# Optimization experiments

Measured on AMD Instinct MI355X. Metric: run time of the kernel, lower is better.

## Reference

```python
import jax, jax.numpy as jnp
import numpy as np


def _minplus(x, W):
    # x: [B, in], W: [out, in] -> y[b,i] = min_j (x[b,j] + W[i,j])
    return jnp.min(x[:, None, :] + W[None, :, :], axis=-1)


def _maxbplus(x, W, b):
    # x: [B, in], W: [out, in], b: [out] -> y[b,i] = max_j (x[b,j] + W[i,j]) + b[i]
    return jnp.max(x[:, None, :] + W[None, :, :], axis=-1) + b


def _basic_block(x, w1, w2, b2, sw1=None, sw2=None, sb2=None):
    out = _maxbplus(_minplus(x, w1), w2, b2)
    sc = x if sw1 is None else _maxbplus(_minplus(x, sw1), sw2, sb2)
    return jnp.minimum(out, sc)


def setup_inputs() -> dict:
    key = jax.random.key(0)
    B, IN, OUT = 1024, 256, 512
    ks = jax.random.split(key, 16)
    s = 0.05
    inp = {
        'x': jax.random.normal(ks[0], (B, IN), jnp.float32),
        # layers 1-3: in==out==IN, no block shortcut params
        'l1_w1': jax.random.normal(ks[1], (IN, IN), jnp.float32) * s,
        'l1_w2': jax.random.normal(ks[2], (IN, IN), jnp.float32) * s,
        'l1_b2': jax.random.normal(ks[3], (IN,), jnp.float32) * s,
        'l2_w1': jax.random.normal(ks[4], (IN, IN), jnp.float32) * s,
        'l2_w2': jax.random.normal(ks[5], (IN, IN), jnp.float32) * s,
        'l2_b2': jax.random.normal(ks[6], (IN,), jnp.float32) * s,
        'l3_w1': jax.random.normal(ks[7], (IN, IN), jnp.float32) * s,
        'l3_w2': jax.random.normal(ks[8], (IN, IN), jnp.float32) * s,
        'l3_b2': jax.random.normal(ks[9], (IN,), jnp.float32) * s,
        # layer 4: IN -> OUT, has block-level shortcut
        'l4_w1': jax.random.normal(ks[10], (OUT, IN), jnp.float32) * s,
        'l4_w2': jax.random.normal(ks[11], (OUT, OUT), jnp.float32) * s,
        'l4_b2': jax.random.normal(ks[12], (OUT,), jnp.float32) * s,
        'l4_sw1': jax.random.normal(ks[13], (OUT, IN), jnp.float32) * s,
        'l4_sw2': jax.random.normal(ks[14], (OUT, OUT), jnp.float32) * s,
        'l4_sb2': jax.random.normal(ks[15], (OUT,), jnp.float32) * s,
    }
    k2 = jax.random.split(jax.random.fold_in(key, 1), 3)
    inp['sc_w1'] = jax.random.normal(k2[0], (OUT, IN), jnp.float32) * s
    inp['sc_w2'] = jax.random.normal(k2[1], (OUT, OUT), jnp.float32) * s
    inp['sc_b2'] = jax.random.normal(k2[2], (OUT,), jnp.float32) * s
    return inp


def reference(x, l1_w1, l1_w2, l1_b2, l2_w1, l2_w2, l2_b2,
              l3_w1, l3_w2, l3_b2, l4_w1, l4_w2, l4_b2,
              l4_sw1, l4_sw2, l4_sb2, sc_w1, sc_w2, sc_b2):
    out = _basic_block(x, l1_w1, l1_w2, l1_b2)            # layer1 (IN->IN)
    out = _basic_block(out, l2_w1, l2_w2, l2_b2)          # layer2
    out = _basic_block(out, l3_w1, l3_w2, l3_b2)          # layer3
    out = _basic_block(out, l4_w1, l4_w2, l4_b2,
                       l4_sw1, l4_sw2, l4_sb2)            # layer4 (IN->OUT)
    sc = _maxbplus(_minplus(x, sc_w1), sc_w2, sc_b2)      # bottleneck shortcut
    return jnp.maximum(out, sc)
```

## Files before the change

kernel.cpp:

```cpp
#include <hip/hip_runtime.h>
#include <math.h>


typedef _Float16 h2 __attribute__((ext_vector_type(2)));
typedef _Float16 h8 __attribute__((ext_vector_type(8)));

template<int M, typename V> __device__ __forceinline__ V rdv(V a, V b) {
    if constexpr (M) return __builtin_elementwise_max(a, b);
    else             return __builtin_elementwise_min(a, b);
}
template<int M> __device__ __forceinline__ _Float16 rd1(_Float16 a, _Float16 b) {
    if constexpr (M) return a > b ? a : b;
    else             return a < b ? a : b;
}
#define XS(v, I0, I1) __builtin_shufflevector(v, v, I0, I1)

struct NetP {
    const float* x;
    const h8 *w11, *w12, *w21, *w22, *w31, *w32;
    const h8 *w41, *w42, *sw1, *sw2, *scw1, *scw2;
    const _Float16 *b12, *b22, *b32, *b42, *sb2, *scb2;
    float* out;
};

template<int ISMAX, int R, int K, bool GOUT>
__device__ __forceinline__ void stage(
    const h8* __restrict__ Wc,
    const _Float16* __restrict__ bias,
    const _Float16* __restrict__ X,
    const _Float16* __restrict__ E1,
    const _Float16* __restrict__ E2,
    _Float16* __restrict__ Y,
    float* __restrict__ gout, int b0,
    _Float16* __restrict__ part)
{
    constexpr int NRG = R / 4;
    constexpr int KS  = 512 / NRG;
    constexpr int NC  = (K / 8) / KS;
    static_assert(NRG * KS == 512, "thread mapping");
    const int tid  = threadIdx.x;
    const int rowg = tid & (NRG - 1);
    const int kq   = tid / NRG;
    const int kc0  = kq * NC;

    const h8* Xc0 = (const h8*)X + kc0;
    const h8* Xc1 = (const h8*)(X + K) + kc0;

    h2 a00, a01, a10, a11, a20, a21, a30, a31;

#define RDA(a, b) rdv<ISMAX>((a), (b))
#define PIECE(J0, J1)                                                   \
    {   h2 xa_ = XS(xa, J0, J1), xb_ = XS(xb, J0, J1); h2 t;            \
        t = XS(w0, J0, J1); a00 = RDA(a00, xa_ + t); a01 = RDA(a01, xb_ + t); \
        t = XS(w1, J0, J1); a10 = RDA(a10, xa_ + t); a11 = RDA(a11, xb_ + t); \
        t = XS(w2, J0, J1); a20 = RDA(a20, xa_ + t); a21 = RDA(a21, xb_ + t); \
        t = XS(w3, J0, J1); a30 = RDA(a30, xa_ + t); a31 = RDA(a31, xb_ + t); }

    {
        h8 xa = Xc0[0], xb = Xc1[0];
        const h8* Wr = Wc + (size_t)kc0 * R + rowg;
        h8 w0 = Wr[0], w1 = Wr[NRG], w2 = Wr[2 * NRG], w3 = Wr[3 * NRG];
        {   h2 xa_ = XS(xa, 0, 1), xb_ = XS(xb, 0, 1); h2 t;
            t = XS(w0, 0, 1); a00 = xa_ + t; a01 = xb_ + t;
            t = XS(w1, 0, 1); a10 = xa_ + t; a11 = xb_ + t;
            t = XS(w2, 0, 1); a20 = xa_ + t; a21 = xb_ + t;
            t = XS(w3, 0, 1); a30 = xa_ + t; a31 = xb_ + t;
        }
        PIECE(2, 3) PIECE(4, 5) PIECE(6, 7)
    }
#pragma unroll 2
    for (int kc = 1; kc < NC; ++kc) {
        h8 xa = Xc0[kc], xb = Xc1[kc];
        const h8* Wr = Wc + (size_t)(kc0 + kc) * R + rowg;
        h8 w0 = Wr[0], w1 = Wr[NRG], w2 = Wr[2 * NRG], w3 = Wr[3 * NRG];
        PIECE(0, 1) PIECE(2, 3) PIECE(4, 5) PIECE(6, 7)
    }
#undef PIECE

    h8 v8;
    v8[0] = rd1<ISMAX>(a00[0], a00[1]); v8[1] = rd1<ISMAX>(a01[0], a01[1]);
    v8[2] = rd1<ISMAX>(a10[0], a10[1]); v8[3] = rd1<ISMAX>(a11[0], a11[1]);
    v8[4] = rd1<ISMAX>(a20[0], a20[1]); v8[5] = rd1<ISMAX>(a21[0], a21[1]);
    v8[6] = rd1<ISMAX>(a30[0], a30[1]); v8[7] = rd1<ISMAX>(a31[0], a31[1]);

    if (kq) *(h8*)(part + ((size_t)(kq - 1) * NRG + rowg) * 8) = v8;
    __syncthreads();
    if (kq == 0) {
#pragma unroll
        for (int qq = 0; qq < KS - 1; ++qq)
            v8 = rdv<ISMAX>(v8, *(const h8*)(part + ((size_t)qq * NRG + rowg) * 8));

#pragma unroll
        for (int i = 0; i < 4; ++i) {
            const int r = rowg + i * NRG;
            _Float16 oc0 = v8[2 * i], oc1 = v8[2 * i + 1];
            if (ISMAX) { _Float16 bi = bias[r]; oc0 += bi; oc1 += bi; }
            if (E1) {
                _Float16 e0 = E1[r], e1 = E1[R + r];
                oc0 = oc0 < e0 ? oc0 : e0; oc1 = oc1 < e1 ? oc1 : e1;
            }
            if (E2) {
                _Float16 e0 = E2[r], e1 = E2[R + r];
                oc0 = oc0 > e0 ? oc0 : e0; oc1 = oc1 > e1 ? oc1 : e1;
            }
            if constexpr (GOUT) {
                gout[(size_t)(b0 + 0) * 512 + r] = (float)oc0;
                gout[(size_t)(b0 + 1) * 512 + r] = (float)oc1;
            } else {
                Y[r] = oc0; Y[R + r] = oc1;
            }
        }
    }
#undef RDA
    __syncthreads();
}

__global__ __launch_bounds__(512) void netf(NetP p)
{
    __shared__ __align__(16) _Float16 X0[2 * 256];
    __shared__ __align__(16) _Float16 B0[2 * 512], B1[2 * 512];
    __shared__ __align__(16) _Float16 B2[2 * 512], B3[2 * 512];
    __shared__ __align__(16) _Float16 part[3584];
    const int tid = threadIdx.x;
    const int b0  = blockIdx.x * 2;

    {
        const int bl = tid >> 8;
        const int k  = tid & 255;
        X0[bl * 256 + k] = (_Float16)p.x[(size_t)(b0 + bl) * 256 + k];
    }
    __syncthreads();

    float* o = p.out;
    stage<0,512,256,false>(p.scw1, nullptr, X0, nullptr, nullptr, B0, o, b0, part);
    stage<1,512,512,false>(p.scw2, p.scb2,  B0, nullptr, nullptr, B1, o, b0, part);
    stage<0,256,256,false>(p.w11, nullptr, X0, nullptr, nullptr, B0, o, b0, part);
    stage<1,256,256,false>(p.w12, p.b12,   B0, X0,      nullptr, B2, o, b0, part);
    stage<0,256,256,false>(p.w21, nullptr, B2, nullptr, nullptr, B0, o, b0, part);
    stage<1,256,256,false>(p.w22, p.b22,   B0, B2,      nullptr, B3, o, b0, part);
    stage<0,256,256,false>(p.w31, nullptr, B3, nullptr, nullptr, B0, o, b0, part);
    stage<1,256,256,false>(p.w32, p.b32,   B0, B3,      nullptr, B2, o, b0, part);
    stage<0,512,256,false>(p.w41, nullptr, B2, nullptr, nullptr, B0, o, b0, part);
    stage<0,512,256,false>(p.sw1, nullptr, B2, nullptr, nullptr, B3, o, b0, part);
    stage<1,512,512,false>(p.w42, p.b42,   B0, nullptr, nullptr, B2, o, b0, part);
    stage<1,512,512,true >(p.sw2, p.sb2,   B3, B2,      B1, nullptr, o, b0, part);
}

struct Prep {
    const float* s[12]; h8* d[12]; int R[12]; int K[12];
    const float* bs[6]; _Float16* bd[6]; int bn[6];
};
__global__ __launch_bounds__(256) void cvtw(Prep p)
{
    const int m = blockIdx.y;
    if (m == 12) {
        if (blockIdx.x != 0) return;
        for (int s = 0; s < 6; ++s)
            for (int i = threadIdx.x; i < p.bn[s]; i += 256)
                p.bd[s][i] = (_Float16)p.bs[s][i];
        return;
    }
    const int R = p.R[m], K = p.K[m];
    const int tilesR = R >> 6;
    const int nt = tilesR * (K >> 6);
    const int t = blockIdx.x;
    if (t >= nt) return;
    const int tr = t % tilesR, tk = t / tilesR;

    __shared__ float s[64][65];
    const int lane = threadIdx.x & 63, ty = threadIdx.x >> 6;
    const float* src = p.s[m];
#pragma unroll
    for (int r = ty; r < 64; r += 4)
        s[r][lane] = src[(size_t)(tr * 64 + r) * K + tk * 64 + lane];
    __syncthreads();
    h8* dst = p.d[m];
#pragma unroll
    for (int c = 0; c < 2; ++c) {
        int cc = ty + c * 4;
        h8 v;
#pragma unroll
        for (int j = 0; j < 8; ++j) v[j] = (_Float16)s[lane][cc * 8 + j];
        dst[(size_t)(tk * 8 + cc) * R + tr * 64 + lane] = v;
    }
}

extern "C" void kernel_launch(void* const* d_in, const int* in_sizes, int n_in,
                              void* d_out, int out_size, void* d_ws, size_t ws_size,
                              hipStream_t stream) {
    (void)in_sizes; (void)n_in; (void)ws_size; (void)out_size;
    const float* fin[19];
    for (int i = 0; i < 19; ++i) fin[i] = (const float*)d_in[i];

    _Float16* hw = (_Float16*)d_ws;

    _Float16* w11c  = hw;
    _Float16* w12c  = hw + 65536;
    _Float16* w21c  = hw + 131072;
    _Float16* w22c  = hw + 196608;
    _Float16* w31c  = hw + 262144;
    _Float16* w32c  = hw + 327680;
    _Float16* w41c  = hw + 393216;
    _Float16* w42c  = hw + 524288;
    _Float16* sw1c  = hw + 786432;
    _Float16* sw2c  = hw + 917504;
    _Float16* scw1c = hw + 1179648;
    _Float16* scw2c = hw + 1310720;
    _Float16* bia   = hw + 1572864;
    _Float16* b12 = bia, *b22 = bia + 256, *b32 = bia + 512;
    _Float16* b42 = bia + 768, *sb2 = bia + 1280, *scb2 = bia + 1792;

    Prep cw;
    const float* wsrc[12] = {fin[1], fin[2], fin[4], fin[5], fin[7], fin[8],
                             fin[10], fin[11], fin[13], fin[14], fin[16], fin[17]};
    _Float16* wdst[12]    = {w11c, w12c, w21c, w22c, w31c, w32c,
                             w41c, w42c, sw1c, sw2c, scw1c, scw2c};
    const int wR[12] = {256,256,256,256,256,256, 512,512,512,512,512,512};
    const int wK[12] = {256,256,256,256,256,256, 256,512,256,512,256,512};
    for (int i = 0; i < 12; ++i) {
        cw.s[i] = wsrc[i]; cw.d[i] = (h8*)wdst[i]; cw.R[i] = wR[i]; cw.K[i] = wK[i];
    }
    const float* bsrc[6] = {fin[3], fin[6], fin[9], fin[12], fin[15], fin[18]};
    _Float16* bdst[6]    = {b12, b22, b32, b42, sb2, scb2};
    const int bn[6]      = {256, 256, 256, 512, 512, 512};
    for (int i = 0; i < 6; ++i) { cw.bs[i] = bsrc[i]; cw.bd[i] = bdst[i]; cw.bn[i] = bn[i]; }

    NetP p;
    p.x   = fin[0];
    p.w11 = (const h8*)w11c; p.w12 = (const h8*)w12c;
    p.w21 = (const h8*)w21c; p.w22 = (const h8*)w22c;
    p.w31 = (const h8*)w31c; p.w32 = (const h8*)w32c;
    p.w41 = (const h8*)w41c; p.w42 = (const h8*)w42c;
    p.sw1 = (const h8*)sw1c; p.sw2 = (const h8*)sw2c;
    p.scw1 = (const h8*)scw1c; p.scw2 = (const h8*)scw2c;
    p.b12 = b12; p.b22 = b22; p.b32 = b32; p.b42 = b42; p.sb2 = sb2; p.scb2 = scb2;
    p.out = (float*)d_out;

    cvtw<<<dim3(64, 13), 256, 0, stream>>>(cw);
    netf<<<dim3(512), dim3(512), 0, stream>>>(p);
}
```

Measured before the change: 82.46 us.

## Process four batch rows per block with 1024 threads, two weight rows per thread

The fused network kernel now handles four batch rows per block instead of two, using 1024 threads per block and 256 blocks. Each thread loads two weight vectors instead of four and applies each to four input rows, so weight loads are reused across more batch rows. This aims to cut global weight traffic per output. In exchange, per-block shared memory and the K-split reduction buffer double, fewer blocks exist, and 1024-thread blocks may limit occupancy and raise synchronization cost.

```diff
diff --git a/kernel.cpp b/kernel.cpp
--- a/kernel.cpp
+++ b/kernel.cpp
@@ -34,54 +34,61 @@
     float* __restrict__ gout, int b0,
     _Float16* __restrict__ part)
 {
-    constexpr int NRG = R / 4;
-    constexpr int KS  = 512 / NRG;
+    constexpr int NRG = R / 2;
+    constexpr int KS  = 1024 / NRG;
     constexpr int NC  = (K / 8) / KS;
-    static_assert(NRG * KS == 512, "thread mapping");
+    static_assert(NRG * KS == 1024, "thread mapping");
     const int tid  = threadIdx.x;
     const int rowg = tid & (NRG - 1);
     const int kq   = tid / NRG;
     const int kc0  = kq * NC;
 
-    const h8* Xc0 = (const h8*)X + kc0;
-    const h8* Xc1 = (const h8*)(X + K) + kc0;
-
-    h2 a00, a01, a10, a11, a20, a21, a30, a31;
+    const h8* X8 = (const h8*)X;
+    const h8* Xc0 = X8 + 0 * (K / 8) + kc0;
+    const h8* Xc1 = X8 + 1 * (K / 8) + kc0;
+    const h8* Xc2 = X8 + 2 * (K / 8) + kc0;
+    const h8* Xc3 = X8 + 3 * (K / 8) + kc0;
+
+    h2 a00, a01, a02, a03, a10, a11, a12, a13;
 
 #define RDA(a, b) rdv<ISMAX>((a), (b))
-#define PIECE(J0, J1)                                                   \
-    {   h2 xa_ = XS(xa, J0, J1), xb_ = XS(xb, J0, J1); h2 t;            \
-        t = XS(w0, J0, J1); a00 = RDA(a00, xa_ + t); a01 = RDA(a01, xb_ + t); \
-        t = XS(w1, J0, J1); a10 = RDA(a10, xa_ + t); a11 = RDA(a11, xb_ + t); \
-        t = XS(w2, J0, J1); a20 = RDA(a20, xa_ + t); a21 = RDA(a21, xb_ + t); \
-        t = XS(w3, J0, J1); a30 = RDA(a30, xa_ + t); a31 = RDA(a31, xb_ + t); }
+#define PIECE(J0, J1)                                                     \
+    {   h2 x0_ = XS(xa, J0, J1), x1_ = XS(xb, J0, J1);                    \
+        h2 x2_ = XS(xc, J0, J1), x3_ = XS(xd, J0, J1); h2 t;              \
+        t = XS(w0, J0, J1);                                               \
+        a00 = RDA(a00, x0_ + t); a01 = RDA(a01, x1_ + t);                 \
+        a02 = RDA(a02, x2_ + t); a03 = RDA(a03, x3_ + t);                 \
+        t = XS(w1, J0, J1);                                               \
+        a10 = RDA(a10, x0_ + t); a11 = RDA(a11, x1_ + t);                 \
+        a12 = RDA(a12, x2_ + t); a13 = RDA(a13, x3_ + t); }
 
     {
-        h8 xa = Xc0[0], xb = Xc1[0];
+        h8 xa = Xc0[0], xb = Xc1[0], xc = Xc2[0], xd = Xc3[0];
         const h8* Wr = Wc + (size_t)kc0 * R + rowg;
-        h8 w0 = Wr[0], w1 = Wr[NRG], w2 = Wr[2 * NRG], w3 = Wr[3 * NRG];
-        {   h2 xa_ = XS(xa, 0, 1), xb_ = XS(xb, 0, 1); h2 t;
-            t = XS(w0, 0, 1); a00 = xa_ + t; a01 = xb_ + t;
-            t = XS(w1, 0, 1); a10 = xa_ + t; a11 = xb_ + t;
-            t = XS(w2, 0, 1); a20 = xa_ + t; a21 = xb_ + t;
-            t = XS(w3, 0, 1); a30 = xa_ + t; a31 = xb_ + t;
+        h8 w0 = Wr[0], w1 = Wr[NRG];
+        {   h2 x0_ = XS(xa, 0, 1), x1_ = XS(xb, 0, 1);
+            h2 x2_ = XS(xc, 0, 1), x3_ = XS(xd, 0, 1); h2 t;
+            t = XS(w0, 0, 1);
+            a00 = x0_ + t; a01 = x1_ + t; a02 = x2_ + t; a03 = x3_ + t;
+            t = XS(w1, 0, 1);
+            a10 = x0_ + t; a11 = x1_ + t; a12 = x2_ + t; a13 = x3_ + t;
         }
         PIECE(2, 3) PIECE(4, 5) PIECE(6, 7)
     }
 #pragma unroll 2
     for (int kc = 1; kc < NC; ++kc) {
-        h8 xa = Xc0[kc], xb = Xc1[kc];
+        h8 xa = Xc0[kc], xb = Xc1[kc], xc = Xc2[kc], xd = Xc3[kc];
         const h8* Wr = Wc + (size_t)(kc0 + kc) * R + rowg;
-        h8 w0 = Wr[0], w1 = Wr[NRG], w2 = Wr[2 * NRG], w3 = Wr[3 * NRG];
+        h8 w0 = Wr[0], w1 = Wr[NRG];
         PIECE(0, 1) PIECE(2, 3) PIECE(4, 5) PIECE(6, 7)
     }
 #undef PIECE
 
     h8 v8;
     v8[0] = rd1<ISMAX>(a00[0], a00[1]); v8[1] = rd1<ISMAX>(a01[0], a01[1]);
-    v8[2] = rd1<ISMAX>(a10[0], a10[1]); v8[3] = rd1<ISMAX>(a11[0], a11[1]);
-    v8[4] = rd1<ISMAX>(a20[0], a20[1]); v8[5] = rd1<ISMAX>(a21[0], a21[1]);
-    v8[6] = rd1<ISMAX>(a30[0], a30[1]); v8[7] = rd1<ISMAX>(a31[0], a31[1]);
+    v8[2] = rd1<ISMAX>(a02[0], a02[1]); v8[3] = rd1<ISMAX>(a03[0], a03[1]);
+    v8[4] = rd1<ISMAX>(a10[0], a10[1]); v8[5] = rd1<ISMAX>(a11[0], a11[1]);
+    v8[6] = rd1<ISMAX>(a12[0], a12[1]); v8[7] = rd1<ISMAX>(a13[0], a13[1]);
 
     if (kq) *(h8*)(part + ((size_t)(kq - 1) * NRG + rowg) * 8) = v8;
     __syncthreads();
@@ -91,23 +98,34 @@
             v8 = rdv<ISMAX>(v8, *(const h8*)(part + ((size_t)qq * NRG + rowg) * 8));
 
 #pragma unroll
-        for (int i = 0; i < 4; ++i) {
+        for (int i = 0; i < 2; ++i) {
             const int r = rowg + i * NRG;
-            _Float16 oc0 = v8[2 * i], oc1 = v8[2 * i + 1];
-            if (ISMAX) { _Float16 bi = bias[r]; oc0 += bi; oc1 += bi; }
+            _Float16 o0 = v8[4 * i + 0], o1 = v8[4 * i + 1];
+            _Float16 o2 = v8[4 * i + 2], o3 = v8[4 * i + 3];
+            if (ISMAX) {
+                _Float16 bi = bias[r];
+                o0 += bi; o1 += bi; o2 += bi; o3 += bi;
+            }
             if (E1) {
-                _Float16 e0 = E1[r], e1 = E1[R + r];
-                oc0 = oc0 < e0 ? oc0 : e0; oc1 = oc1 < e1 ? oc1 : e1;
+                _Float16 e0 = E1[0 * R + r], e1 = E1[1 * R + r];
+                _Float16 e2 = E1[2 * R + r], e3 = E1[3 * R + r];
+                o0 = o0 < e0 ? o0 : e0; o1 = o1 < e1 ? o1 : e1;
+                o2 = o2 < e2 ? o2 : e2; o3 = o3 < e3 ? o3 : e3;
             }
             if (E2) {
-                _Float16 e0 = E2[r], e1 = E2[R + r];
-                oc0 = oc0 > e0 ? oc0 : e0; oc1 = oc1 > e1 ? oc1 : e1;
+                _Float16 e0 = E2[0 * R + r], e1 = E2[1 * R + r];
+                _Float16 e2 = E2[2 * R + r], e3 = E2[3 * R + r];
+                o0 = o0 > e0 ? o0 : e0; o1 = o1 > e1 ? o1 : e1;
+                o2 = o2 > e2 ? o2 : e2; o3 = o3 > e3 ? o3 : e3;
             }
             if constexpr (GOUT) {
-                gout[(size_t)(b0 + 0) * 512 + r] = (float)oc0;
-                gout[(size_t)(b0 + 1) * 512 + r] = (float)oc1;
+                gout[(size_t)(b0 + 0) * 512 + r] = (float)o0;
+                gout[(size_t)(b0 + 1) * 512 + r] = (float)o1;
+                gout[(size_t)(b0 + 2) * 512 + r] = (float)o2;
+                gout[(size_t)(b0 + 3) * 512 + r] = (float)o3;
             } else {
-                Y[r] = oc0; Y[R + r] = oc1;
+                Y[0 * R + r] = o0; Y[1 * R + r] = o1;
+                Y[2 * R + r] = o2; Y[3 * R + r] = o3;
             }
         }
     }
@@ -115,14 +133,14 @@
     __syncthreads();
 }
 
-__global__ __launch_bounds__(512) void netf(NetP p)
+__global__ __launch_bounds__(1024) void netf(NetP p)
 {
-    __shared__ __align__(16) _Float16 X0[2 * 256];
-    __shared__ __align__(16) _Float16 B0[2 * 512], B1[2 * 512];
-    __shared__ __align__(16) _Float16 B2[2 * 512], B3[2 * 512];
-    __shared__ __align__(16) _Float16 part[3584];
+    __shared__ __align__(16) _Float16 X0[4 * 256];
+    __shared__ __align__(16) _Float16 B0[4 * 512], B1[4 * 512];
+    __shared__ __align__(16) _Float16 B2[4 * 512], B3[4 * 512];
+    __shared__ __align__(16) _Float16 part[7168];
     const int tid = threadIdx.x;
-    const int b0  = blockIdx.x * 2;
+    const int b0  = blockIdx.x * 4;
 
     {
         const int bl = tid >> 8;
@@ -237,5 +255,5 @@
     p.out = (float*)d_out;
 
     cvtw<<<dim3(64, 13), 256, 0, stream>>>(cw);
-    netf<<<dim3(512), dim3(512), 0, stream>>>(p);
-}
+    netf<<<dim3(256), dim3(1024), 0, stream>>>(p);
+}
```

New measurement: 86.42 us. +4.8%, slower.
